# Optimization experiments

Hardware: AMD Instinct MI355X
Metric: run time of the kernel (lower is better)

## Reference

```python
import jax, jax.numpy as jnp
import numpy as np

N_SEQ, N_RES, C_M = 512, 256, 256
C_OUTER, C_Z = 32, 128
LN_EPS = 1e-5
NORM_EPS = 1e-3


def setup_inputs() -> dict:
    key = jax.random.key(0)
    ks = jax.random.split(key, 6)
    f32 = jnp.float32
    return {
        "act": jax.random.normal(ks[0], (N_SEQ, N_RES, C_M), f32),
        "mask": jnp.ones((N_SEQ, N_RES), f32),
        # LayerNorm params (create_scale=True, create_offset=True)
        "ln_scale": jnp.ones((C_M,), f32),
        "ln_offset": jnp.zeros((C_M,), f32),
        # left/right projections, 'linear' (VarianceScaling fan_in scale=1)
        "left_w": (jax.random.normal(ks[1], (C_M, C_OUTER), f32) / np.float32(np.sqrt(C_M))),
        "left_b": jnp.zeros((C_OUTER,), f32),
        "right_w": (jax.random.normal(ks[2], (C_M, C_OUTER), f32) / np.float32(np.sqrt(C_M))),
        "right_b": jnp.zeros((C_OUTER,), f32),
        # output_w: VarianceScaling(scale=2.0, fan_in) over (c_outer, c_outer) input dims
        "output_w": (jax.random.normal(ks[3], (C_OUTER, C_OUTER, C_Z), f32)
                     * np.float32(np.sqrt(2.0 / (C_OUTER * C_OUTER)))),
        "output_b": jnp.zeros((C_Z,), f32),
    }


def reference(act, mask, ln_scale, ln_offset, left_w, left_b, right_w, right_b,
              output_w, output_b):
    # LayerNorm over last axis
    mu = jnp.mean(act, axis=-1, keepdims=True)
    var = jnp.var(act, axis=-1, keepdims=True)
    x = (act - mu) * jax.lax.rsqrt(var + LN_EPS) * ln_scale + ln_offset

    m = mask[..., None]  # [N_seq, N_res, 1]
    left = m * (jnp.einsum('abm,mc->abc', x, left_w) + left_b)    # [A,B,Co]
    right = m * (jnp.einsum('abm,me->abe', x, right_w) + right_b)  # [A,D,Co]

    # mean outer product: sum over MSA depth a -> [B, D, Co, Co]
    op = jnp.einsum('abc,ade->bdce', left, right)
    out = jnp.einsum('bdce,cef->bdf', op, output_w) + output_b  # [B, D, Cz]

    # normalization by pairwise mask counts
    norm = jnp.einsum('ab,ad->bd', mask, mask)[..., None]  # [B, D, 1]
    return out / (NORM_EPS + norm)
```

## Files before the change

### kernel.cpp

```cpp
#include <hip/hip_runtime.h>
#include <hip/hip_bf16.h>
#include <stdint.h>

typedef short bf16x8 __attribute__((ext_vector_type(8)));
typedef float f32x4 __attribute__((ext_vector_type(4)));
typedef unsigned short u16x4 __attribute__((ext_vector_type(4)));
typedef unsigned short u16x8 __attribute__((ext_vector_type(8)));

#define GLOAD16(g, l) __builtin_amdgcn_global_load_lds( \
    (const __attribute__((address_space(1))) void*)(g), \
    (__attribute__((address_space(3))) void*)(l), 16, 0, 0)

__device__ __forceinline__ unsigned short f2bf(float f) {
  unsigned u = __float_as_uint(f);
  unsigned r = (u + 0x7fffu + ((u >> 16) & 1u)) >> 16;
  return (unsigned short)r;
}

__global__ __launch_bounds__(256) void prep_k(
    const float* __restrict__ lw, const float* __restrict__ rw,
    const float* __restrict__ ow, unsigned short* __restrict__ Wt,
    unsigned short* __restrict__ wfragG) {
  int idx = blockIdx.x * 256 + threadIdx.x;
  if (idx < 131072) {
    int f = idx >> 10, k2 = idx & 1023;
    int e = k2 >> 5, c = k2 & 31;
    Wt[idx] = f2bf(ow[(size_t)((c << 5) + e) * 128 + f]);
  }
  if (idx < 16384) {
    int frag = idx >> 9, lane = (idx >> 3) & 63, j = idx & 7;
    int wc = frag >> 4, ni = (frag >> 3) & 1, kk = frag & 7;
    int mrow = lane & 15, g = lane >> 4;
    int c = wc * 32 + ni * 16 + mrow;
    int k = kk * 32 + g * 8 + j;
    wfragG[idx] = f2bf(c < 32 ? lw[k * 32 + c] : rw[k * 32 + (c - 32)]);
  }
}

__global__ __launch_bounds__(256) void norm_k(const float* __restrict__ mask,
                                              float* __restrict__ nrm) {
  int b = blockIdx.x, d = threadIdx.x;
  float s = 0.f;
  #pragma unroll 8
  for (int a = 0; a < 512; ++a)
    s += mask[a * 256 + b] * mask[a * 256 + d];
  nrm[(b << 8) + d] = s;
}

__global__ __launch_bounds__(256, 4) void ln_proj(
    const float* __restrict__ act, const float* __restrict__ mask,
    const float* __restrict__ lns, const float* __restrict__ lno,
    const float* __restrict__ lb, const float* __restrict__ rb,
    const unsigned short* __restrict__ wfragG,
    unsigned short* __restrict__ Lt, unsigned short* __restrict__ Rt) {
  __shared__ char smem[32768];
  const int tid = threadIdx.x;
  const int lane = tid & 63;
  const int w = tid >> 6;
  const int b = blockIdx.y;
  const int a0 = blockIdx.x << 6;
  const int l = tid & 15;
  const int rg = tid >> 4;

  f32x4 sc[4], of[4];
  #pragma unroll
  for (int j = 0; j < 4; ++j) {
    sc[j] = *(const f32x4*)(lns + (l << 4) + (j << 2));
    of[j] = *(const f32x4*)(lno + (l << 4) + (j << 2));
  }

  #pragma unroll
  for (int i = 0; i < 4; ++i) {
    const int r = rg + (i << 4);
    const float* src = act + ((size_t)(a0 + r) * 256 + b) * 256 + (l << 4);
    f32x4 xv[4];
    #pragma unroll
    for (int j = 0; j < 4; ++j) xv[j] = *(const f32x4*)(src + (j << 2));
    float s = 0.f, sq = 0.f;
    #pragma unroll
    for (int j = 0; j < 4; ++j) {
      f32x4 v = xv[j];
      s += v[0] + v[1] + v[2] + v[3];
      sq += v[0] * v[0] + v[1] * v[1] + v[2] * v[2] + v[3] * v[3];
    }
    s += __shfl_xor(s, 1); sq += __shfl_xor(sq, 1);
    s += __shfl_xor(s, 2); sq += __shfl_xor(sq, 2);
    s += __shfl_xor(s, 4); sq += __shfl_xor(sq, 4);
    s += __shfl_xor(s, 8); sq += __shfl_xor(sq, 8);
    const float mu = s * (1.f / 256.f);
    const float rs = rsqrtf(sq * (1.f / 256.f) - mu * mu + 1e-5f);
    #pragma unroll
    for (int hh = 0; hh < 2; ++hh) {
      u16x8 pk;
      #pragma unroll
      for (int j2 = 0; j2 < 2; ++j2) {
        const int j = (hh << 1) + j2;
        #pragma unroll
        for (int e = 0; e < 4; ++e)
          pk[(j2 << 2) + e] = f2bf((xv[j][e] - mu) * rs * sc[j][e] + of[j][e]);
      }
      const int c = (l << 1) + hh;
      *(u16x8*)(smem + (r << 9) + ((c ^ (r & 7)) << 4)) = pk;
    }
  }
  __syncthreads();

  const int wr = w >> 1, wc = w & 1;
  const int mrow = lane & 15, g = lane >> 4;
  f32x4 acc[2][2];
  #pragma unroll
  for (int i = 0; i < 2; ++i)
    #pragma unroll
    for (int jj = 0; jj < 2; ++jj) acc[i][jj] = (f32x4){0.f, 0.f, 0.f, 0.f};
  #pragma unroll
  for (int kk = 0; kk < 8; ++kk) {
    bf16x8 af[2], bfr[2];
    #pragma unroll
    for (int mi = 0; mi < 2; ++mi) {
      const int row = (wr << 5) + (mi << 4) + mrow;
      af[mi] = *(const bf16x8*)(smem + (row << 9) + ((((kk << 2) + g) ^ (row & 7)) << 4));
    }
    #pragma unroll
    for (int ni = 0; ni < 2; ++ni)
      bfr[ni] = *(const bf16x8*)(wfragG + (size_t)((((wc << 1) + ni) << 3) + kk) * 512 + (lane << 3));
    #pragma unroll
    for (int mi = 0; mi < 2; ++mi)
      #pragma unroll
      for (int ni = 0; ni < 2; ++ni)
        acc[mi][ni] = __builtin_amdgcn_mfma_f32_16x16x32_bf16(af[mi], bfr[ni], acc[mi][ni], 0, 0, 0);
  }
  __syncthreads();

  #pragma unroll
  for (int ni = 0; ni < 2; ++ni) {
    const int c = (wc << 5) + (ni << 4) + mrow;
    const float bias = (wc == 0) ? lb[(ni << 4) + mrow] : rb[(ni << 4) + mrow];
    #pragma unroll
    for (int mi = 0; mi < 2; ++mi) {
      const int aB = (wr << 5) + (mi << 4) + (g << 2);
      u16x4 pk;
      #pragma unroll
      for (int qq = 0; qq < 4; ++qq) {
        const float mk = mask[(size_t)(a0 + aB + qq) * 256 + b];
        pk[qq] = f2bf((acc[mi][ni][qq] + bias) * mk);
      }
      *(u16x4*)(smem + (c << 7) + ((((aB >> 3) & 7) ^ (c & 7)) << 4) + ((aB & 7) << 1)) = pk;
    }
  }
  __syncthreads();

  #pragma unroll
  for (int s = 0; s < 2; ++s) {
    const int c = (w << 4) + (s << 3) + (lane >> 3);
    const int gr = lane & 7;
    const u16x8 v = *(const u16x8*)(smem + (c << 7) + ((gr ^ (c & 7)) << 4));
    unsigned short* dst = (c < 32) ? Lt : Rt;
    *(u16x8*)(dst + (size_t)(b * 32 + (c & 31)) * 512 + a0 + (gr << 3)) = v;
  }
}

__global__ __launch_bounds__(512, 2) void gemm_fused(
    const unsigned short* __restrict__ Lt, const unsigned short* __restrict__ Rt,
    const unsigned short* __restrict__ Wt, const float* __restrict__ nrm,
    const float* __restrict__ outb, float* __restrict__ out) {
  __shared__ char smem[131072];
  const int tid = threadIdx.x;
  const int lane = tid & 63;
  const int w = tid >> 6;
  const int wr = w >> 2, wc = w & 3;
  const int mrow = lane & 15, g = lane >> 4;

  const int bid = blockIdx.x;
  const int xcd = bid & 7, jj_ = bid >> 3;
  const int mb = ((jj_ >> 5) << 3) | (jj_ & 7);
  const int nb = (xcd << 2) | ((jj_ >> 3) & 3);
  const int m0i = mb << 8, n0i = nb << 8;

  const int scol = (((tid & 7) ^ ((tid >> 3) & 7)) << 3);

  f32x4 acc[8][4];
  #pragma unroll
  for (int i = 0; i < 8; ++i)
    #pragma unroll
    for (int jj = 0; jj < 4; ++jj) acc[i][jj] = (f32x4){0.f, 0.f, 0.f, 0.f};

  auto STG = [&](const unsigned short* gsrc, int baserow, int dstoff, int kt) {
    GLOAD16(gsrc + ((size_t)(baserow + (tid >> 3)) << 9) + (kt << 6) + scol,
            smem + dstoff + (tid << 4));
  };

  STG(Rt, n0i, 32768, 0);        STG(Rt, n0i + 64, 40960, 0);
  STG(Rt, n0i + 128, 49152, 0);  STG(Rt, n0i + 192, 57344, 0);
  STG(Lt, m0i, 0, 0);            STG(Lt, m0i + 128, 16384, 0);
  STG(Lt, m0i + 64, 8192, 0);    STG(Lt, m0i + 192, 24576, 0);
  asm volatile("s_waitcnt vmcnt(2)" ::: "memory");
  __builtin_amdgcn_s_barrier();

  #pragma unroll 1
  for (int t = 0; t < 8; ++t) {
    const int cbuf = (t & 1) << 16;
    const int nbuf = ((t + 1) & 1) << 16;
    const int k1 = t + 1;
    const bool pfe = (t < 7);
    bf16x8 bfr[4][2];
    #pragma unroll
    for (int p = 0; p < 4; ++p) {
      const int h = p >> 1, kk = p & 1;
      bf16x8 af[4];
      #pragma unroll
      for (int mi_ = 0; mi_ < 4; ++mi_) {
        af[mi_] = *(const bf16x8*)(smem + cbuf + (((wr << 1) + h) << 13) +
                                   (((mi_ << 4) + mrow) << 7) +
                                   ((((kk << 2) + g) ^ (mrow & 7)) << 4));
      }
      if (p < 2) {
        #pragma unroll
        for (int ni = 0; ni < 4; ++ni)
          bfr[ni][p] = *(const bf16x8*)(smem + cbuf + 32768 + (wc << 13) +
                                        (((ni << 4) + mrow) << 7) +
                                        ((((p << 2) + g) ^ (mrow & 7)) << 4));
      }
      if (pfe) {
        if (p == 0)      { STG(Rt, n0i, nbuf + 32768, k1);       STG(Rt, n0i + 64, nbuf + 40960, k1); }
        else if (p == 1) { STG(Rt, n0i + 128, nbuf + 49152, k1); STG(Rt, n0i + 192, nbuf + 57344, k1); }
        else if (p == 2) { STG(Lt, m0i, nbuf, k1);               STG(Lt, m0i + 128, nbuf + 16384, k1); }
        else             { STG(Lt, m0i + 64, nbuf + 8192, k1);   STG(Lt, m0i + 192, nbuf + 24576, k1); }
      }
      asm volatile("s_waitcnt lgkmcnt(0)" ::: "memory");
      __builtin_amdgcn_sched_barrier(0);
      __builtin_amdgcn_s_setprio(1);
      #pragma unroll
      for (int mi_ = 0; mi_ < 4; ++mi_)
        #pragma unroll
        for (int ni = 0; ni < 4; ++ni)
          acc[(h << 2) + mi_][ni] = __builtin_amdgcn_mfma_f32_16x16x32_bf16(
              af[mi_], bfr[ni][kk], acc[(h << 2) + mi_][ni], 0, 0, 0);
      __builtin_amdgcn_s_setprio(0);
      if (p == 1) {
        if (t < 7) asm volatile("s_waitcnt vmcnt(4)" ::: "memory");
        else       asm volatile("s_waitcnt vmcnt(0)" ::: "memory");
      } else if (p == 3 && pfe) {
        asm volatile("s_waitcnt vmcnt(2)" ::: "memory");
      }
      __builtin_amdgcn_s_barrier();
    }
  }

  #pragma unroll
  for (int mi = 0; mi < 8; ++mi) {
    #pragma unroll
    for (int ni = 0; ni < 4; ++ni) {
      const int p = (((wr << 2) + (mi >> 1)) << 3) | ((wc << 1) + (ni >> 1));
      const int ow_ = ((ni & 1) << 10) + (mrow << 6) + ((mi & 1) << 5) + (g << 3);
      u16x4 pk;
      #pragma unroll
      for (int qq = 0; qq < 4; ++qq) pk[qq] = f2bf(acc[mi][ni][qq]);
      *(u16x4*)(smem + (p << 11) + (ow_ ^ ((p & 7) << 4) ^ (((ow_ >> 7) & 7) << 4))) = pk;
    }
  }
  __syncthreads();

  f32x4 invn[4];
  #pragma unroll
  for (int pg = 0; pg < 4; ++pg) {
    const int bb = (mb << 3) + (pg << 1) + (g >> 1);
    const f32x4 nv = *(const f32x4*)(nrm + (bb << 8) + (nb << 3) + ((g & 1) << 2));
    #pragma unroll
    for (int qq = 0; qq < 4; ++qq) invn[pg][qq] = __builtin_amdgcn_rcpf(1e-3f + nv[qq]);
  }

  const int f0 = w << 4;
  f32x4 acc2[4];
  #pragma unroll
  for (int i = 0; i < 4; ++i) acc2[i] = (f32x4){0.f, 0.f, 0.f, 0.f};
  const unsigned short* wrow = Wt + (size_t)(f0 + mrow) * 1024;
  #pragma unroll 8
  for (int kk2 = 0; kk2 < 32; ++kk2) {
    const bf16x8 b2 = *(const bf16x8*)(wrow + (kk2 << 5) + (g << 3));
    const int orr = (kk2 << 6) + (g << 4);
    #pragma unroll
    for (int pg = 0; pg < 4; ++pg) {
      const int prow = (pg << 4) + mrow;
      const bf16x8 a2 = *(const bf16x8*)(smem + (prow << 11) +
          (orr ^ ((prow & 7) << 4) ^ (((orr >> 7) & 7) << 4)));
      acc2[pg] = __builtin_amdgcn_mfma_f32_16x16x32_bf16(a2, b2, acc2[pg], 0, 0, 0);
    }
  }

  const float ob_ = outb[f0 + mrow];
  #pragma unroll
  for (int pg = 0; pg < 4; ++pg) {
    #pragma unroll
    for (int qq = 0; qq < 4; ++qq) {
      const int p = (pg << 4) + (g << 2) + qq;
      const int bb = (mb << 3) + (p >> 3);
      const int dd = (nb << 3) + (p & 7);
      out[(size_t)((bb << 8) + dd) * 128 + f0 + mrow] = (acc2[pg][qq] + ob_) * invn[pg][qq];
    }
  }
}

extern "C" void kernel_launch(void* const* d_in, const int* in_sizes, int n_in,
                              void* d_out, int out_size, void* d_ws, size_t ws_size,
                              hipStream_t stream) {
  const float* act = (const float*)d_in[0];
  const float* mask = (const float*)d_in[1];
  const float* lns = (const float*)d_in[2];
  const float* lno = (const float*)d_in[3];
  const float* lw = (const float*)d_in[4];
  const float* lb = (const float*)d_in[5];
  const float* rw = (const float*)d_in[6];
  const float* rbv = (const float*)d_in[7];
  const float* ow = (const float*)d_in[8];
  const float* ob = (const float*)d_in[9];
  float* out = (float*)d_out;
  char* ws = (char*)d_ws;

  unsigned short* Lt = (unsigned short*)(ws);
  unsigned short* Rt = (unsigned short*)(ws + 8388608);
  unsigned short* Wt = (unsigned short*)(ws + 16777216);
  unsigned short* wfragG = (unsigned short*)(ws + 17039360);
  float* nrm = (float*)(ws + 17072128);

  hipLaunchKernelGGL(prep_k, dim3(512), dim3(256), 0, stream, lw, rw, ow, Wt, wfragG);
  hipLaunchKernelGGL(norm_k, dim3(256), dim3(256), 0, stream, mask, nrm);
  hipLaunchKernelGGL(ln_proj, dim3(8, 256), dim3(256), 0, stream,
                     act, mask, lns, lno, lb, rbv, wfragG, Lt, Rt);
  hipLaunchKernelGGL(gemm_fused, dim3(1024), dim3(512), 0, stream,
                     Lt, Rt, Wt, nrm, ob, out);
}
```

Baseline: 158.6 us.

## Use 32x32 MFMA tiles with whole-tile double buffering and merge prep kernels

The first GEMM stage of the fused kernel moves from 16x16x32 MFMAs to 32x32x16 bf16 MFMAs with f32x16 accumulators. This raises math per LDS fragment load. The software pipeline now loads whole k-tiles two steps ahead, with per-tile barriers, instead of interleaving partial prefetches inside each k-step. The accumulator write-back to shared memory is rewritten for the new fragment layout. Separately, the weight prep and mask-norm kernels are merged into one launch to save a kernel launch. The cost is less overlap within a k-step, plus possible register-pressure changes.

```diff
diff --git a/kernel.cpp b/kernel.cpp
--- a/kernel.cpp
+++ b/kernel.cpp
@@ -4,6 +4,7 @@
 
 typedef short bf16x8 __attribute__((ext_vector_type(8)));
 typedef float f32x4 __attribute__((ext_vector_type(4)));
+typedef float f32x16 __attribute__((ext_vector_type(16)));
 typedef unsigned short u16x4 __attribute__((ext_vector_type(4)));
 typedef unsigned short u16x8 __attribute__((ext_vector_type(8)));
 
@@ -17,34 +18,35 @@
   return (unsigned short)r;
 }
 
-__global__ __launch_bounds__(256) void prep_k(
+__global__ __launch_bounds__(256) void prep_norm_k(
     const float* __restrict__ lw, const float* __restrict__ rw,
-    const float* __restrict__ ow, unsigned short* __restrict__ Wt,
-    unsigned short* __restrict__ wfragG) {
-  int idx = blockIdx.x * 256 + threadIdx.x;
-  if (idx < 131072) {
-    int f = idx >> 10, k2 = idx & 1023;
-    int e = k2 >> 5, c = k2 & 31;
-    Wt[idx] = f2bf(ow[(size_t)((c << 5) + e) * 128 + f]);
-  }
-  if (idx < 16384) {
-    int frag = idx >> 9, lane = (idx >> 3) & 63, j = idx & 7;
-    int wc = frag >> 4, ni = (frag >> 3) & 1, kk = frag & 7;
-    int mrow = lane & 15, g = lane >> 4;
-    int c = wc * 32 + ni * 16 + mrow;
-    int k = kk * 32 + g * 8 + j;
-    wfragG[idx] = f2bf(c < 32 ? lw[k * 32 + c] : rw[k * 32 + (c - 32)]);
-  }
-}
-
-__global__ __launch_bounds__(256) void norm_k(const float* __restrict__ mask,
-                                              float* __restrict__ nrm) {
-  int b = blockIdx.x, d = threadIdx.x;
-  float s = 0.f;
-  #pragma unroll 8
-  for (int a = 0; a < 512; ++a)
-    s += mask[a * 256 + b] * mask[a * 256 + d];
-  nrm[(b << 8) + d] = s;
+    const float* __restrict__ ow, const float* __restrict__ mask,
+    unsigned short* __restrict__ Wt, unsigned short* __restrict__ wfragG,
+    float* __restrict__ nrm) {
+  const int bid = blockIdx.x;
+  if (bid < 512) {
+    int idx = bid * 256 + threadIdx.x;
+    if (idx < 131072) {
+      int f = idx >> 10, k2 = idx & 1023;
+      int e = k2 >> 5, c = k2 & 31;
+      Wt[idx] = f2bf(ow[(size_t)((c << 5) + e) * 128 + f]);
+    }
+    if (idx < 16384) {
+      int frag = idx >> 9, lane = (idx >> 3) & 63, j = idx & 7;
+      int wc = frag >> 4, ni = (frag >> 3) & 1, kk = frag & 7;
+      int mrow = lane & 15, g = lane >> 4;
+      int c = wc * 32 + ni * 16 + mrow;
+      int k = kk * 32 + g * 8 + j;
+      wfragG[idx] = f2bf(c < 32 ? lw[k * 32 + c] : rw[k * 32 + (c - 32)]);
+    }
+  } else {
+    const int b = bid - 512, d = threadIdx.x;
+    float s = 0.f;
+    #pragma unroll 8
+    for (int a = 0; a < 512; ++a)
+      s += mask[a * 256 + b] * mask[a * 256 + d];
+    nrm[(b << 8) + d] = s;
+  }
 }
 
 __global__ __launch_bounds__(256, 4) void ln_proj(
@@ -168,6 +170,7 @@
   const int lane = tid & 63;
   const int w = tid >> 6;
   const int wr = w >> 2, wc = w & 3;
+  const int l31 = lane & 31, hi = lane >> 5;
   const int mrow = lane & 15, g = lane >> 4;
 
   const int bid = blockIdx.x;
@@ -178,84 +181,82 @@
 
   const int scol = (((tid & 7) ^ ((tid >> 3) & 7)) << 3);
 
-  f32x4 acc[8][4];
-  #pragma unroll
-  for (int i = 0; i < 8; ++i)
-    #pragma unroll
-    for (int jj = 0; jj < 4; ++jj) acc[i][jj] = (f32x4){0.f, 0.f, 0.f, 0.f};
+  f32x16 acc32[4][2];
+  #pragma unroll
+  for (int i = 0; i < 4; ++i)
+    #pragma unroll
+    for (int jj = 0; jj < 2; ++jj)
+      #pragma unroll
+      for (int e = 0; e < 16; ++e) acc32[i][jj][e] = 0.f;
 
   auto STG = [&](const unsigned short* gsrc, int baserow, int dstoff, int kt) {
     GLOAD16(gsrc + ((size_t)(baserow + (tid >> 3)) << 9) + (kt << 6) + scol,
             smem + dstoff + (tid << 4));
   };
-
-  STG(Rt, n0i, 32768, 0);        STG(Rt, n0i + 64, 40960, 0);
-  STG(Rt, n0i + 128, 49152, 0);  STG(Rt, n0i + 192, 57344, 0);
-  STG(Lt, m0i, 0, 0);            STG(Lt, m0i + 128, 16384, 0);
-  STG(Lt, m0i + 64, 8192, 0);    STG(Lt, m0i + 192, 24576, 0);
-  asm volatile("s_waitcnt vmcnt(2)" ::: "memory");
+  auto STGALL = [&](int buf, int kt) {
+    STG(Rt, n0i, buf + 32768, kt);        STG(Rt, n0i + 64, buf + 40960, kt);
+    STG(Rt, n0i + 128, buf + 49152, kt);  STG(Rt, n0i + 192, buf + 57344, kt);
+    STG(Lt, m0i, buf + 0, kt);            STG(Lt, m0i + 64, buf + 8192, kt);
+    STG(Lt, m0i + 128, buf + 16384, kt);  STG(Lt, m0i + 192, buf + 24576, kt);
+  };
+
+  STGALL(0, 0);
+  STGALL(65536, 1);
+  asm volatile("s_waitcnt vmcnt(8)" ::: "memory");
   __builtin_amdgcn_s_barrier();
 
   #pragma unroll 1
   for (int t = 0; t < 8; ++t) {
-    const int cbuf = (t & 1) << 16;
-    const int nbuf = ((t + 1) & 1) << 16;
-    const int k1 = t + 1;
-    const bool pfe = (t < 7);
-    bf16x8 bfr[4][2];
-    #pragma unroll
-    for (int p = 0; p < 4; ++p) {
-      const int h = p >> 1, kk = p & 1;
-      bf16x8 af[4];
-      #pragma unroll
-      for (int mi_ = 0; mi_ < 4; ++mi_) {
-        af[mi_] = *(const bf16x8*)(smem + cbuf + (((wr << 1) + h) << 13) +
-                                   (((mi_ << 4) + mrow) << 7) +
-                                   ((((kk << 2) + g) ^ (mrow & 7)) << 4));
-      }
-      if (p < 2) {
+    const char* bufp = smem + ((t & 1) << 16);
+    #pragma unroll
+    for (int kk = 0; kk < 4; ++kk) {
+      bf16x8 af[4], bfv[2];
+      #pragma unroll
+      for (int Mg = 0; Mg < 4; ++Mg) {
+        const int row = (wr << 7) + (Mg << 5) + l31;
+        af[Mg] = *(const bf16x8*)(bufp + (row << 7) +
+                                  ((((kk << 1) + hi) ^ (row & 7)) << 4));
+      }
+      #pragma unroll
+      for (int Ng = 0; Ng < 2; ++Ng) {
+        const int row = (wc << 6) + (Ng << 5) + l31;
+        bfv[Ng] = *(const bf16x8*)(bufp + 32768 + (row << 7) +
+                                   ((((kk << 1) + hi) ^ (row & 7)) << 4));
+      }
+      #pragma unroll
+      for (int Mg = 0; Mg < 4; ++Mg)
         #pragma unroll
-        for (int ni = 0; ni < 4; ++ni)
-          bfr[ni][p] = *(const bf16x8*)(smem + cbuf + 32768 + (wc << 13) +
-                                        (((ni << 4) + mrow) << 7) +
-                                        ((((p << 2) + g) ^ (mrow & 7)) << 4));
-      }
-      if (pfe) {
-        if (p == 0)      { STG(Rt, n0i, nbuf + 32768, k1);       STG(Rt, n0i + 64, nbuf + 40960, k1); }
-        else if (p == 1) { STG(Rt, n0i + 128, nbuf + 49152, k1); STG(Rt, n0i + 192, nbuf + 57344, k1); }
-        else if (p == 2) { STG(Lt, m0i, nbuf, k1);               STG(Lt, m0i + 128, nbuf + 16384, k1); }
-        else             { STG(Lt, m0i + 64, nbuf + 8192, k1);   STG(Lt, m0i + 192, nbuf + 24576, k1); }
-      }
-      asm volatile("s_waitcnt lgkmcnt(0)" ::: "memory");
-      __builtin_amdgcn_sched_barrier(0);
-      __builtin_amdgcn_s_setprio(1);
-      #pragma unroll
-      for (int mi_ = 0; mi_ < 4; ++mi_)
+        for (int Ng = 0; Ng < 2; ++Ng)
+          acc32[Mg][Ng] = __builtin_amdgcn_mfma_f32_32x32x16_bf16(
+              af[Mg], bfv[Ng], acc32[Mg][Ng], 0, 0, 0);
+    }
+    if (t < 6) {
+      __builtin_amdgcn_s_barrier();
+      STGALL((t & 1) << 16, t + 2);
+      asm volatile("s_waitcnt vmcnt(8)" ::: "memory");
+      __builtin_amdgcn_s_barrier();
+    } else if (t == 6) {
+      asm volatile("s_waitcnt vmcnt(0)" ::: "memory");
+      __builtin_amdgcn_s_barrier();
+    }
+  }
+  __syncthreads();
+
+  #pragma unroll
+  for (int Mg = 0; Mg < 4; ++Mg) {
+    #pragma unroll
+    for (int Ng = 0; Ng < 2; ++Ng) {
+      const int p = (((wr << 2) + Mg) << 3) | ((wc << 1) + Ng);
+      #pragma unroll
+      for (int q = 0; q < 4; ++q) {
+        const int c0 = (q << 3) + (hi << 2);
+        const int ow_ = (l31 << 6) + (c0 << 1);
+        u16x4 pk;
         #pragma unroll
-        for (int ni = 0; ni < 4; ++ni)
-          acc[(h << 2) + mi_][ni] = __builtin_amdgcn_mfma_f32_16x16x32_bf16(
-              af[mi_], bfr[ni][kk], acc[(h << 2) + mi_][ni], 0, 0, 0);
-      __builtin_amdgcn_s_setprio(0);
-      if (p == 1) {
-        if (t < 7) asm volatile("s_waitcnt vmcnt(4)" ::: "memory");
-        else       asm volatile("s_waitcnt vmcnt(0)" ::: "memory");
-      } else if (p == 3 && pfe) {
-        asm volatile("s_waitcnt vmcnt(2)" ::: "memory");
-      }
-      __builtin_amdgcn_s_barrier();
-    }
-  }
-
-  #pragma unroll
-  for (int mi = 0; mi < 8; ++mi) {
-    #pragma unroll
-    for (int ni = 0; ni < 4; ++ni) {
-      const int p = (((wr << 2) + (mi >> 1)) << 3) | ((wc << 1) + (ni >> 1));
-      const int ow_ = ((ni & 1) << 10) + (mrow << 6) + ((mi & 1) << 5) + (g << 3);
-      u16x4 pk;
-      #pragma unroll
-      for (int qq = 0; qq < 4; ++qq) pk[qq] = f2bf(acc[mi][ni][qq]);
-      *(u16x4*)(smem + (p << 11) + (ow_ ^ ((p & 7) << 4) ^ (((ow_ >> 7) & 7) << 4))) = pk;
+        for (int j = 0; j < 4; ++j) pk[j] = f2bf(acc32[Mg][Ng][(q << 2) + j]);
+        *(u16x4*)(smem + (p << 11) +
+                  (ow_ ^ ((p & 7) << 4) ^ (((ow_ >> 7) & 7) << 4))) = pk;
+      }
     }
   }
   __syncthreads();
@@ -322,8 +323,8 @@
   unsigned short* wfragG = (unsigned short*)(ws + 17039360);
   float* nrm = (float*)(ws + 17072128);
 
-  hipLaunchKernelGGL(prep_k, dim3(512), dim3(256), 0, stream, lw, rw, ow, Wt, wfragG);
-  hipLaunchKernelGGL(norm_k, dim3(256), dim3(256), 0, stream, mask, nrm);
+  hipLaunchKernelGGL(prep_norm_k, dim3(768), dim3(256), 0, stream,
+                     lw, rw, ow, mask, Wt, wfragG, nrm);
   hipLaunchKernelGGL(ln_proj, dim3(8, 256), dim3(256), 0, stream,
                      act, mask, lns, lno, lb, rbv, wfragG, Lt, Rt);
   hipLaunchKernelGGL(gemm_fused, dim3(1024), dim3(512), 0, stream,
```

New measurement: 156.7 us. About the same (-1.2%).
